# Performance work log

Hardware: AMD Instinct MI355X
Metric: run time of the kernel (lower is better)

Reference implementation:

```python
import jax, jax.numpy as jnp
import numpy as np

N_HEADS = 32
N_KV_HEADS = 8
HEAD_DIM = 128


def setup_inputs() -> dict:
    key = jax.random.key(0)
    ks = jax.random.split(key, 7)
    B, S, D = 2, 2048, 4096
    scale = 0.02
    x = jax.random.normal(ks[0], (B, S, D), dtype=jnp.float32)
    wq = jax.random.normal(ks[1], (D, D), dtype=jnp.float32) * scale
    wk = jax.random.normal(ks[2], (N_KV_HEADS * HEAD_DIM, D), dtype=jnp.float32) * scale
    wv = jax.random.normal(ks[3], (N_KV_HEADS * HEAD_DIM, D), dtype=jnp.float32) * scale
    wo = jax.random.normal(ks[4], (D, D), dtype=jnp.float32) * scale
    # RoPE frequencies: theta = 10000^{-2i/d}, angles = pos * theta
    inv_freq = 1.0 / (10000.0 ** (jnp.arange(0, HEAD_DIM, 2, dtype=jnp.float32) / HEAD_DIM))
    angles = jnp.arange(S, dtype=jnp.float32)[:, None] * inv_freq[None, :]  # (S, HEAD_DIM//2)
    freqs_cos = jnp.cos(angles)
    freqs_sin = jnp.sin(angles)
    # causal additive mask (0 on/below diagonal, -inf above)
    neg_inf = jnp.finfo(jnp.float32).min
    mask = jnp.where(jnp.triu(jnp.ones((S, S), dtype=bool), k=1), neg_inf, 0.0)[None, None]
    return {"x": x, "wq": wq, "wk": wk, "wv": wv, "wo": wo,
            "freqs_cos": freqs_cos, "freqs_sin": freqs_sin, "mask": mask,
            "start_pos": 0}


def _apply_rope(t, cos, sin):
    # t: (B, S, H, D); cos/sin: (S, D//2) -> broadcast (1, S, 1, D//2)
    b, s, h, d = t.shape
    tr = t.reshape(b, s, h, d // 2, 2)
    te, to = tr[..., 0], tr[..., 1]
    c = cos[None, :, None, :]
    si = sin[None, :, None, :]
    out = jnp.stack([te * c - to * si, te * si + to * c], axis=-1)
    return out.reshape(b, s, h, d)


def reference(x, wq, wk, wv, wo, freqs_cos, freqs_sin, mask, start_pos):
    b, s, d = x.shape
    n_rep = N_HEADS // N_KV_HEADS
    xq = (x @ wq.T).reshape(b, s, N_HEADS, HEAD_DIM)
    xk = (x @ wk.T).reshape(b, s, N_KV_HEADS, HEAD_DIM)
    xv = (x @ wv.T).reshape(b, s, N_KV_HEADS, HEAD_DIM)
    xq = _apply_rope(xq, freqs_cos, freqs_sin)
    xk = _apply_rope(xk, freqs_cos, freqs_sin)
    # repeat_kv: (B, S, Hkv, D) -> (B, S, Hkv*n_rep, D)
    keys = jnp.broadcast_to(xk[:, :, :, None, :], (b, s, N_KV_HEADS, n_rep, HEAD_DIM)).reshape(b, s, N_HEADS, HEAD_DIM)
    values = jnp.broadcast_to(xv[:, :, :, None, :], (b, s, N_KV_HEADS, n_rep, HEAD_DIM)).reshape(b, s, N_HEADS, HEAD_DIM)
    q = xq.transpose(0, 2, 1, 3)       # (B, H, S, D)
    k = keys.transpose(0, 2, 1, 3)
    v = values.transpose(0, 2, 1, 3)
    scores = jnp.einsum("bhqd,bhkd->bhqk", q, k) / np.sqrt(HEAD_DIM).astype(np.float32)
    scores = scores + mask
    probs = jax.nn.softmax(scores.astype(jnp.float32), axis=-1).astype(q.dtype)
    out = jnp.einsum("bhqk,bhkd->bhqd", probs, v)
    out = out.transpose(0, 2, 1, 3).reshape(b, s, N_HEADS * HEAD_DIM)
    return out @ wo.T
```

## Files before the change

kernel.cpp:

```cpp
#include <hip/hip_runtime.h>
#include <cstdint>
#include <cstddef>

#define B_  2
#define S_  2048
#define D_  4096
#define NH  32
#define NKV 8
#define HD  128

typedef unsigned short u16;
typedef unsigned int   u32;
typedef __attribute__((ext_vector_type(8))) short short8;
typedef __attribute__((ext_vector_type(4))) float f32x4;
typedef __attribute__((ext_vector_type(4))) u32   u32x4;

__device__ __forceinline__ u16 f2bf(float f) {
  u32 u = __float_as_uint(f);
  u32 r = (u + 0x7FFFu + ((u >> 16) & 1u)) >> 16;
  return (u16)r;
}
__device__ __forceinline__ float bf2f(u32 lo16) {
  return __uint_as_float(lo16 << 16);
}
__device__ __forceinline__ u32 cvtpk_bf16(float lo, float hi) {
  u32 r;
  asm("v_cvt_pk_bf16_f32 %0, %1, %2" : "=v"(r) : "v"(lo), "v"(hi));
  return r;
}
__device__ __forceinline__ short8 u32x4_to_short8(u32x4 v) {
  union { u32x4 a; short8 b; } u; u.a = v; return u.b;
}
__device__ __forceinline__ void load_lds16(const void* g, void* lds) {
  __builtin_amdgcn_global_load_lds(
      (const __attribute__((address_space(1))) u32*)g,
      (__attribute__((address_space(3))) u32*)lds, 16, 0, 0);
}

__global__ __launch_bounds__(256) void cvt_all(
    const float* __restrict__ x, const float* __restrict__ wq,
    const float* __restrict__ wk, const float* __restrict__ wv,
    const float* __restrict__ wo, u16* __restrict__ Xb, u16* __restrict__ Wqb,
    u16* __restrict__ Wkb, u16* __restrict__ Wvb, u16* __restrict__ Wob) {
  long i = (long)blockIdx.x * 256 + threadIdx.x;
  const float* src; u16* dst; long off;
  if (i < 2097152L)      { src = x;  dst = Xb;  off = i; }
  else if (i < 4194304L) { src = wq; dst = Wqb; off = i - 2097152L; }
  else if (i < 4718592L) { src = wk; dst = Wkb; off = i - 4194304L; }
  else if (i < 5242880L) { src = wv; dst = Wvb; off = i - 4718592L; }
  else                   { src = wo; dst = Wob; off = i - 5242880L; }
  const float4* s = (const float4*)src + off * 2;
  float4 a = s[0], b = s[1];
  uint4 o;
  o.x = (u32)f2bf(a.x) | ((u32)f2bf(a.y) << 16);
  o.y = (u32)f2bf(a.z) | ((u32)f2bf(a.w) << 16);
  o.z = (u32)f2bf(b.x) | ((u32)f2bf(b.y) << 16);
  o.w = (u32)f2bf(b.z) | ((u32)f2bf(b.w) << 16);
  *((uint4*)dst + off) = o;
}

template <int MODE, bool ROPE>
__global__ __launch_bounds__(512, 2)
void gemm256(const u16* __restrict__ A, const u16* __restrict__ Bw,
             void* __restrict__ Cout, int M, int N, int K, int Hh,
             const float* __restrict__ fc, const float* __restrict__ fs) {
  const int tid = threadIdx.x, lid = tid & 63, w = tid >> 6;
  const int lr = lid & 15, lg = lid >> 4;
  const int wm = w >> 2, wn = w & 3;

  int lin = blockIdx.y * gridDim.x + blockIdx.x;
  int bm, bn;
  if (gridDim.x == 16 && gridDim.y == 16) {
    int xcd = lin & 7, idx = lin >> 3;
    bm = ((xcd & 3) * 4 + (idx >> 3)) * 256;
    bn = ((xcd >> 2) * 8 + (idx & 7)) * 256;
  } else {
    bm = blockIdx.y * 256;
    bn = blockIdx.x * 256;
  }

  __shared__ __align__(16) u16 Al[2][2][128 * 64];
  __shared__ __align__(16) u16 Bl[2][2][128 * 64];

  f32x4 acc[8][4];
#pragma unroll
  for (int i = 0; i < 8; ++i)
#pragma unroll
    for (int j = 0; j < 4; ++j) acc[i][j] = (f32x4){0.f, 0.f, 0.f, 0.f};

#define STG_AQ(BUF, QH, KT)                                                    \
  do {                                                                         \
    _Pragma("unroll")                                                          \
    for (int j_ = 0; j_ < 2; ++j_) {                                           \
      int c_ = j_ * 512 + tid;                                                 \
      int idx_ = c_ >> 3, cb_ = c_ & 7;                                        \
      int sr_ = bm + ((idx_ & 64) << 1) + (QH) * 64 + (idx_ & 63);             \
      int sc_ = (cb_ ^ idx_) & 7;                                              \
      load_lds16(A + (size_t)sr_ * K + (KT) + sc_ * 8, &Al[BUF][QH][c_ * 8]);  \
    }                                                                          \
  } while (0)
#define STG_BN(BUF, NHh, KT)                                                   \
  do {                                                                         \
    _Pragma("unroll")                                                          \
    for (int j_ = 0; j_ < 2; ++j_) {                                           \
      int c_ = j_ * 512 + tid;                                                 \
      int idx_ = c_ >> 3, cb_ = c_ & 7;                                        \
      int sr_ = bn + ((idx_ & 96) << 1) + (NHh) * 32 + (idx_ & 31);            \
      int sc_ = (cb_ ^ idx_) & 7;                                              \
      load_lds16(Bw + (size_t)sr_ * K + (KT) + sc_ * 8, &Bl[BUF][NHh][c_ * 8]);\
    }                                                                          \
  } while (0)
#define READ_AQ(BUF, MH)                                                       \
  do {                                                                         \
    _Pragma("unroll")                                                          \
    for (int mi_ = 0; mi_ < 4; ++mi_) {                                        \
      int ix_ = wm * 64 + mi_ * 16 + lr;                                       \
      _Pragma("unroll")                                                        \
      for (int ks_ = 0; ks_ < 2; ++ks_)                                        \
        aq[mi_][ks_] = *(const short8*)&Al[BUF][MH]                            \
            [ix_ * 64 + (((ks_ * 4 + lg) ^ ix_) & 7) * 8];                     \
    }                                                                          \
  } while (0)
#define READ_BN(BUF, NHh, ARR)                                                 \
  do {                                                                         \
    _Pragma("unroll")                                                          \
    for (int ni_ = 0; ni_ < 2; ++ni_) {                                        \
      int ix_ = wn * 32 + ni_ * 16 + lr;                                       \
      _Pragma("unroll")                                                        \
      for (int ks_ = 0; ks_ < 2; ++ks_)                                        \
        ARR[ni_][ks_] = *(const short8*)&Bl[BUF][NHh]                          \
            [ix_ * 64 + (((ks_ * 4 + lg) ^ ix_) & 7) * 8];                     \
    }                                                                          \
  } while (0)
#define MFMA16(MH, NHh, ARR)                                                   \
  do {                                                                         \
    __builtin_amdgcn_s_setprio(1);                                             \
    _Pragma("unroll")                                                          \
    for (int ks_ = 0; ks_ < 2; ++ks_)                                          \
      _Pragma("unroll")                                                        \
      for (int mi_ = 0; mi_ < 4; ++mi_)                                        \
        _Pragma("unroll")                                                      \
        for (int ni_ = 0; ni_ < 2; ++ni_)                                      \
          acc[(MH) * 4 + mi_][(NHh) * 2 + ni_] =                               \
              __builtin_amdgcn_mfma_f32_16x16x32_bf16(                         \
                  aq[mi_][ks_], ARR[ni_][ks_],                                 \
                  acc[(MH) * 4 + mi_][(NHh) * 2 + ni_], 0, 0, 0);              \
    __builtin_amdgcn_s_setprio(0);                                             \
  } while (0)
#define BAR()   __builtin_amdgcn_s_barrier()
#define SCHED0() __builtin_amdgcn_sched_barrier(0)
#define LGKM0() asm volatile("s_waitcnt lgkmcnt(0)" ::: "memory")

  const int nt = K >> 6;
  const int niter = nt >> 1;

  STG_AQ(0, 0, 0); STG_BN(0, 0, 0); STG_BN(0, 1, 0); STG_AQ(0, 1, 0);
  STG_AQ(1, 0, 64); STG_BN(1, 0, 64); STG_BN(1, 1, 64);
  asm volatile("s_waitcnt vmcnt(6)" ::: "memory");
  BAR();

  short8 aq[4][2], bn0[2][2], bn1[2][2];
  for (int j = 0; j < niter; ++j) {
    const bool pf = (j + 1 < niter);
    const int k1 = (2 * j + 1) << 6, k2 = (2 * j + 2) << 6, k3 = (2 * j + 3) << 6;

    READ_AQ(0, 0); READ_BN(0, 0, bn0);
    STG_AQ(1, 1, k1);
    SCHED0(); BAR(); LGKM0(); SCHED0();
    MFMA16(0, 0, bn0); BAR();

    READ_BN(0, 1, bn1);
    if (pf) STG_AQ(0, 0, k2);
    SCHED0(); BAR(); LGKM0(); SCHED0();
    MFMA16(0, 1, bn1); BAR();

    READ_AQ(0, 1);
    if (pf) STG_BN(0, 0, k2);
    SCHED0(); BAR(); LGKM0(); SCHED0();
    MFMA16(1, 0, bn0); BAR();

    if (pf) STG_BN(0, 1, k2);
    SCHED0(); BAR(); LGKM0(); SCHED0();
    MFMA16(1, 1, bn1);
    if (pf) asm volatile("s_waitcnt vmcnt(6)" ::: "memory");
    else    asm volatile("s_waitcnt vmcnt(0)" ::: "memory");
    BAR();

    READ_AQ(1, 0); READ_BN(1, 0, bn0);
    if (pf) STG_AQ(0, 1, k2);
    SCHED0(); BAR(); LGKM0(); SCHED0();
    MFMA16(0, 0, bn0); BAR();

    READ_BN(1, 1, bn1);
    if (pf) STG_AQ(1, 0, k3);
    SCHED0(); BAR(); LGKM0(); SCHED0();
    MFMA16(0, 1, bn1); BAR();

    READ_AQ(1, 1);
    if (pf) STG_BN(1, 0, k3);
    SCHED0(); BAR(); LGKM0(); SCHED0();
    MFMA16(1, 0, bn0); BAR();

    if (pf) STG_BN(1, 1, k3);
    SCHED0(); BAR(); LGKM0(); SCHED0();
    MFMA16(1, 1, bn1);
    if (pf) {
      asm volatile("s_waitcnt vmcnt(6)" ::: "memory");
      BAR();
    }
  }
#undef STG_AQ
#undef STG_BN
#undef READ_AQ
#undef READ_BN
#undef MFMA16
#undef BAR
#undef SCHED0
#undef LGKM0

#pragma unroll
  for (int mi = 0; mi < 8; ++mi)
#pragma unroll
    for (int ni = 0; ni < 4; ++ni)
#pragma unroll
      for (int v = 0; v < 4; ++v) {
        int m = bm + wm * 128 + mi * 16 + lg * 4 + v;
        int n = bn + wn * 64 + ni * 16 + lr;
        float val = acc[mi][ni][v];
        if (ROPE) {
          int srow = m & (S_ - 1);
          int j = (n & (HD - 1)) >> 1;
          float c = fc[(size_t)srow * 64 + j];
          float s = fs[(size_t)srow * 64 + j];
          float partner = __shfl_xor(val, 1);
          val = (n & 1) ? (val * c + partner * s) : (val * c - partner * s);
          val *= (0.08838834764831845f * 1.44269504088896340f);
        }
        if (MODE == 0) {
          ((float*)Cout)[(size_t)m * N + n] = val;
        } else if (MODE == 1) {
          int b = m >> 11, s = m & (S_ - 1), hh = n >> 7, d = n & (HD - 1);
          ((u16*)Cout)[(((size_t)(b * Hh + hh)) * S_ + s) * HD + d] = f2bf(val);
        } else {
          int b = m >> 11, s = m & (S_ - 1), hh = n >> 7, d = n & (HD - 1);
          ((u16*)Cout)[(((size_t)(b * Hh + hh)) * HD + d) * S_ + s] = f2bf(val);
        }
      }
}

__global__ __launch_bounds__(256)
void gemm_kv(const u16* __restrict__ Xb, const u16* __restrict__ Wk,
             const u16* __restrict__ Wv, u16* __restrict__ Kr, u16* __restrict__ Vt,
             const float* __restrict__ fc, const float* __restrict__ fs) {
  const int tid = threadIdx.x;
  const int lid = tid & 63, w = tid >> 6;
  const int lr = lid & 15, lg = lid >> 4;
  const int wm = w >> 1, wn = w & 1;
  const int zz = blockIdx.z;
  const u16* Bw = zz ? Wv : Wk;
  const int K = D_;

  const int gx = gridDim.x;
  const int nwg = gx * gridDim.y;
  const int lin = blockIdx.y * gx + blockIdx.x;
  const int cpx = nwg >> 3;
  const int lin2 = (lin & 7) * cpx + (lin >> 3);
  const int bm = (lin2 / gx) * 128, bn = (lin2 % gx) * 128;

  __shared__ __align__(16) u16 Al[128 * 64];
  __shared__ __align__(16) u16 Bl[128 * 64];
  f32x4 acc[4][4];
#pragma unroll
  for (int i = 0; i < 4; ++i)
#pragma unroll
    for (int j = 0; j < 4; ++j) acc[i][j] = (f32x4){0.f, 0.f, 0.f, 0.f};

  for (int k0 = 0; k0 < K; k0 += 64) {
    __syncthreads();
#pragma unroll
    for (int i = 0; i < 4; ++i) {
      int c = i * 256 + tid;
      int row = c >> 3, cb = c & 7;
      int cbs = (cb ^ row) & 7;
      load_lds16(Xb + (size_t)(bm + row) * K + k0 + cbs * 8, &Al[c * 8]);
    }
#pragma unroll
    for (int i = 0; i < 4; ++i) {
      int c = i * 256 + tid;
      int row = c >> 3, cb = c & 7;
      int cbs = (cb ^ row) & 7;
      load_lds16(Bw + (size_t)(bn + row) * K + k0 + cbs * 8, &Bl[c * 8]);
    }
    __syncthreads();
#pragma unroll
    for (int ks = 0; ks < 2; ++ks) {
      short8 af[4], bf[4];
#pragma unroll
      for (int mi = 0; mi < 4; ++mi) {
        int row = wm * 64 + mi * 16 + lr;
        af[mi] = *(const short8*)&Al[row * 64 + (((ks * 4 + lg) ^ row) & 7) * 8];
      }
#pragma unroll
      for (int ni = 0; ni < 4; ++ni) {
        int row = wn * 64 + ni * 16 + lr;
        bf[ni] = *(const short8*)&Bl[row * 64 + (((ks * 4 + lg) ^ row) & 7) * 8];
      }
#pragma unroll
      for (int mi = 0; mi < 4; ++mi)
#pragma unroll
        for (int ni = 0; ni < 4; ++ni)
          acc[mi][ni] = __builtin_amdgcn_mfma_f32_16x16x32_bf16(af[mi], bf[ni], acc[mi][ni], 0, 0, 0);
    }
  }
#pragma unroll
  for (int mi = 0; mi < 4; ++mi)
#pragma unroll
    for (int ni = 0; ni < 4; ++ni)
#pragma unroll
      for (int v = 0; v < 4; ++v) {
        int m = bm + wm * 64 + mi * 16 + lg * 4 + v;
        int n = bn + wn * 64 + ni * 16 + lr;
        float val = acc[mi][ni][v];
        int b = m >> 11, s = m & (S_ - 1), hh = n >> 7, d = n & (HD - 1);
        if (zz == 0) {
          int j = d >> 1;
          float c = fc[(size_t)s * 64 + j];
          float sn = fs[(size_t)s * 64 + j];
          float partner = __shfl_xor(val, 1);
          val = (n & 1) ? (val * c + partner * sn) : (val * c - partner * sn);
          Kr[(((size_t)(b * NKV + hh)) * S_ + s) * HD + d] = f2bf(val);
        } else {
          int x = s & 31;
          int sp = (s & ~31) | (((x >> 2) & 3) * 8 + ((x >> 4) & 1) * 4 + (x & 3));
          Vt[(((size_t)(b * NKV + hh)) * HD + d) * S_ + sp] = f2bf(val);
        }
      }
}

__global__ __launch_bounds__(512, 4)
void attn_k(const u16* __restrict__ Qr, const u16* __restrict__ Kr,
            const u16* __restrict__ Vt, u16* __restrict__ Ao) {
  const int xp = blockIdx.x, h = blockIdx.y, b = blockIdx.z;
  const int kvh = h >> 2;
  const int tid = threadIdx.x, lid = tid & 63, w = tid >> 6;
  const int lr = lid & 15, lg = lid >> 4;
  __shared__ __align__(16) u16 Kl[2][64 * 128];
  __shared__ __align__(16) u16 Vl[2][128 * 64];

  const size_t qbase = ((size_t)(b * NH + h)) * S_ * HD;
  const size_t kbase = ((size_t)(b * NKV + kvh)) * S_ * HD;
  const size_t vbase = ((size_t)(b * NKV + kvh)) * HD * S_;

#define STAGE(BUF, KT)                                                              \
  do {                                                                              \
    _Pragma("unroll")                                                               \
    for (int i_ = 0; i_ < 2; ++i_) {                                                \
      int c_ = i_ * 512 + tid;                                                      \
      int row_ = c_ >> 4, cb_ = c_ & 15;                                            \
      int cbs_ = (cb_ & 8) | ((cb_ ^ row_) & 7);                                    \
      load_lds16(&Kr[kbase + (size_t)((KT) + row_) * HD + cbs_ * 8],                \
                 &Kl[BUF][(i_ * 512 + w * 64) * 8]);                                \
    }                                                                               \
    _Pragma("unroll")                                                               \
    for (int i_ = 0; i_ < 2; ++i_) {                                                \
      int c_ = i_ * 512 + tid;                                                      \
      int d_ = c_ >> 3, cb_ = c_ & 7;                                               \
      int cbs_ = (cb_ ^ d_) & 7;                                                    \
      load_lds16(&Vt[vbase + (size_t)d_ * S_ + (KT) + cbs_ * 8],                    \
                 &Vl[BUF][(i_ * 512 + w * 64) * 8]);                                \
    }                                                                               \
  } while (0)

  for (int part = 0; part < 2; ++part) {
    const int qi = part ? xp : (15 - xp);
    const int qb = qi * 128;
    const int ntiles = qi * 2 + 2;
    const int q_abs = qb + w * 16 + lr;

    short8 qf[4];
#pragma unroll
    for (int ks = 0; ks < 4; ++ks)
      qf[ks] = *(const short8*)&Qr[qbase + (size_t)q_abs * HD + ks * 32 + lg * 8];

    float m2 = -3.0e38f, osum = 0.f;
    f32x4 oacc[8];
#pragma unroll
    for (int nd = 0; nd < 8; ++nd) oacc[nd] = (f32x4){0.f, 0.f, 0.f, 0.f};

    STAGE(0, 0);
    __syncthreads();
    int cur = 0;

    for (int t = 0; t < ntiles; ++t) {
      const int kt = t * 64;
      if (t + 1 < ntiles) STAGE(cur ^ 1, kt + 64);

      f32x4 sc[4];
#pragma unroll
      for (int ni = 0; ni < 4; ++ni) sc[ni] = (f32x4){0.f, 0.f, 0.f, 0.f};
      __builtin_amdgcn_s_setprio(1);
#pragma unroll
      for (int ks = 0; ks < 4; ++ks) {
#pragma unroll
        for (int ni = 0; ni < 4; ++ni) {
          int row = ni * 16 + lr;
          int ch = ks * 4 + lg;
          int chs = (ch & 8) | ((ch ^ row) & 7);
          short8 kf = *(const short8*)&Kl[cur][row * 128 + chs * 8];
          sc[ni] = __builtin_amdgcn_mfma_f32_16x16x32_bf16(kf, qf[ks], sc[ni], 0, 0, 0);
        }
      }
      __builtin_amdgcn_s_setprio(0);

      const bool edge = (kt + 64 > qb);
      if (edge) {
#pragma unroll
        for (int ni = 0; ni < 4; ++ni)
#pragma unroll
          for (int v = 0; v < 4; ++v) {
            int kv = kt + ni * 16 + lg * 4 + v;
            if (kv > q_abs) sc[ni][v] = -3.0e38f;
          }
      }
      float mab = fmaxf(fmaxf(fmaxf(sc[0][0], sc[0][1]), fmaxf(sc[0][2], sc[0][3])),
                        fmaxf(fmaxf(sc[1][0], sc[1][1]), fmaxf(sc[1][2], sc[1][3])));
      float mcd = fmaxf(fmaxf(fmaxf(sc[2][0], sc[2][1]), fmaxf(sc[2][2], sc[2][3])),
                        fmaxf(fmaxf(sc[3][0], sc[3][1]), fmaxf(sc[3][2], sc[3][3])));
      float mx = fmaxf(mab, mcd);
      mx = fmaxf(mx, __shfl_xor(mx, 16));
      mx = fmaxf(mx, __shfl_xor(mx, 32));

      if (__any(mx > m2 + 8.0f)) {
        float mnew = fmaxf(m2, mx);
        float fr = exp2f(m2 - mnew);
        m2 = mnew;
        osum *= fr;
#pragma unroll
        for (int nd = 0; nd < 8; ++nd) oacc[nd] *= fr;
      }

      u32x4 pw0, pw1;
      float ps = 0.f;
#pragma unroll
      for (int ni = 0; ni < 4; ++ni) {
#pragma unroll
        for (int p = 0; p < 2; ++p) {
          float e0 = exp2f(sc[ni][2 * p] - m2);
          float e1 = exp2f(sc[ni][2 * p + 1] - m2);
          ps += e0 + e1;
          u32 pk = cvtpk_bf16(e0, e1);
          if (ni < 2) pw0[(ni & 1) * 2 + p] = pk;
          else        pw1[(ni & 1) * 2 + p] = pk;
        }
      }
      osum += ps;
      const short8 pf0 = u32x4_to_short8(pw0);
      const short8 pf1 = u32x4_to_short8(pw1);

      __builtin_amdgcn_s_setprio(1);
#pragma unroll
      for (int ks = 0; ks < 2; ++ks) {
        const short8 pfk = ks ? pf1 : pf0;
#pragma unroll
        for (int nd = 0; nd < 8; ++nd) {
          int rowv = nd * 16 + lr;
          int ch = ks * 4 + lg;
          short8 vf = *(const short8*)&Vl[cur][rowv * 64 + ((ch ^ rowv) & 7) * 8];
          oacc[nd] = __builtin_amdgcn_mfma_f32_16x16x32_bf16(vf, pfk, oacc[nd], 0, 0, 0);
        }
      }
      __builtin_amdgcn_s_setprio(0);
      __syncthreads();
      cur ^= 1;
    }

    float os = osum;
    os += __shfl_xor(os, 16);
    os += __shfl_xor(os, 32);
    const float inv = 1.0f / os;
    const size_t orow = ((size_t)(b * S_ + q_abs)) * D_ + h * HD;
    u32* AoW = (u32*)Ao;
#pragma unroll
    for (int nd = 0; nd < 8; ++nd) {
#pragma unroll
      for (int p = 0; p < 2; ++p) {
        u32 pk = cvtpk_bf16(oacc[nd][2 * p] * inv, oacc[nd][2 * p + 1] * inv);
        AoW[(orow + nd * 16 + lg * 4 + 2 * p) >> 1] = pk;
      }
    }
  }
#undef STAGE
}

extern "C" void kernel_launch(void* const* d_in, const int* in_sizes, int n_in,
                              void* d_out, int out_size, void* d_ws, size_t ws_size,
                              hipStream_t stream) {
  const float* x  = (const float*)d_in[0];
  const float* wq = (const float*)d_in[1];
  const float* wk = (const float*)d_in[2];
  const float* wv = (const float*)d_in[3];
  const float* wo = (const float*)d_in[4];
  const float* fc = (const float*)d_in[5];
  const float* fs = (const float*)d_in[6];

  const size_t SZ_X  = (size_t)B_ * S_ * D_ * 2;
  const size_t SZ_WQ = (size_t)D_ * D_ * 2;
  const size_t SZ_WK = (size_t)NKV * HD * D_ * 2;
  char* ws = (char*)d_ws;
  u16* Xb  = (u16*)(ws);
  u16* Wqb = (u16*)(ws + SZ_X);
  u16* Wkb = (u16*)(ws + SZ_X + SZ_WQ);
  u16* Wvb = (u16*)(ws + SZ_X + SZ_WQ + SZ_WK);
  u16* Wob = (u16*)(ws + SZ_X + SZ_WQ + 2 * SZ_WK);
  u16* Qr  = (u16*)(ws + SZ_X + 2 * SZ_WQ + 2 * SZ_WK);
  u16* Kr  = (u16*)(ws + 2 * SZ_X + 2 * SZ_WQ + 2 * SZ_WK);
  u16* Vt  = (u16*)(ws + 2 * SZ_X + 2 * SZ_WQ + 3 * SZ_WK);
  u16* Ao  = (u16*)(ws + 2 * SZ_X + 2 * SZ_WQ + 4 * SZ_WK);
  const size_t NEEDED = 3 * SZ_X + 2 * SZ_WQ + 4 * SZ_WK;
  if (ws_size < NEEDED) return;

  cvt_all<<<28672, 256, 0, stream>>>(x, wq, wk, wv, wo, Xb, Wqb, Wkb, Wvb, Wob);

  gemm256<1, true><<<dim3(16, 16), 512, 0, stream>>>(
      Xb, Wqb, Qr, B_ * S_, D_, D_, NH, fc, fs);
  gemm_kv<<<dim3(8, 32, 2), 256, 0, stream>>>(Xb, Wkb, Wvb, Kr, Vt, fc, fs);

  attn_k<<<dim3(8, NH, B_), 512, 0, stream>>>(Qr, Kr, Vt, Ao);

  gemm256<0, false><<<dim3(16, 16), 512, 0, stream>>>(
      Ao, Wob, d_out, B_ * S_, D_, D_, 0, nullptr, nullptr);
}
```

Before: 499.0 us.

## Process two 16-row query subtiles per warp in attention to reuse K/V fragments

Each warp now handles 32 query rows instead of 16, so the attention block covers 256 queries, and the grid is halved to 4 blocks per head. Every K and V fragment read from LDS feeds two MFMAs instead of one, halving LDS traffic and staging per query. In exchange each thread holds more registers (doubled accumulators and scores), occupancy drops to two blocks per CU, and with only 256 blocks the load balance across CUs gets coarser.

```diff
diff --git a/kernel.cpp b/kernel.cpp
--- a/kernel.cpp
+++ b/kernel.cpp
@@ -337,7 +337,7 @@
       }
 }
 
-__global__ __launch_bounds__(512, 4)
+__global__ __launch_bounds__(512, 2)
 void attn_k(const u16* __restrict__ Qr, const u16* __restrict__ Kr,
             const u16* __restrict__ Vt, u16* __restrict__ Ao) {
   const int xp = blockIdx.x, h = blockIdx.y, b = blockIdx.z;
@@ -372,20 +372,24 @@
   } while (0)
 
   for (int part = 0; part < 2; ++part) {
-    const int qi = part ? xp : (15 - xp);
-    const int qb = qi * 128;
-    const int ntiles = qi * 2 + 2;
-    const int q_abs = qb + w * 16 + lr;
-
-    short8 qf[4];
-#pragma unroll
-    for (int ks = 0; ks < 4; ++ks)
-      qf[ks] = *(const short8*)&Qr[qbase + (size_t)q_abs * HD + ks * 32 + lg * 8];
-
-    float m2 = -3.0e38f, osum = 0.f;
-    f32x4 oacc[8];
-#pragma unroll
-    for (int nd = 0; nd < 8; ++nd) oacc[nd] = (f32x4){0.f, 0.f, 0.f, 0.f};
+    const int pi = part ? xp : (7 - xp);
+    const int qb = pi * 256;
+    const int ntiles = pi * 4 + 4;
+    const int qa0 = qb + w * 32 + lr;
+
+    short8 qf[2][4];
+#pragma unroll
+    for (int mi = 0; mi < 2; ++mi)
+#pragma unroll
+      for (int ks = 0; ks < 4; ++ks)
+        qf[mi][ks] = *(const short8*)&Qr[qbase + (size_t)(qa0 + mi * 16) * HD + ks * 32 + lg * 8];
+
+    float m2[2] = {-3.0e38f, -3.0e38f}, osum[2] = {0.f, 0.f};
+    f32x4 oacc[2][8];
+#pragma unroll
+    for (int mi = 0; mi < 2; ++mi)
+#pragma unroll
+      for (int nd = 0; nd < 8; ++nd) oacc[mi][nd] = (f32x4){0.f, 0.f, 0.f, 0.f};
 
     STAGE(0, 0);
     __syncthreads();
@@ -395,9 +399,11 @@
       const int kt = t * 64;
       if (t + 1 < ntiles) STAGE(cur ^ 1, kt + 64);
 
-      f32x4 sc[4];
-#pragma unroll
-      for (int ni = 0; ni < 4; ++ni) sc[ni] = (f32x4){0.f, 0.f, 0.f, 0.f};
+      f32x4 sc[2][4];
+#pragma unroll
+      for (int mi = 0; mi < 2; ++mi)
+#pragma unroll
+        for (int ni = 0; ni < 4; ++ni) sc[mi][ni] = (f32x4){0.f, 0.f, 0.f, 0.f};
       __builtin_amdgcn_s_setprio(1);
 #pragma unroll
       for (int ks = 0; ks < 4; ++ks) {
@@ -407,66 +413,83 @@
           int ch = ks * 4 + lg;
           int chs = (ch & 8) | ((ch ^ row) & 7);
           short8 kf = *(const short8*)&Kl[cur][row * 128 + chs * 8];
-          sc[ni] = __builtin_amdgcn_mfma_f32_16x16x32_bf16(kf, qf[ks], sc[ni], 0, 0, 0);
+#pragma unroll
+          for (int mi = 0; mi < 2; ++mi)
+            sc[mi][ni] = __builtin_amdgcn_mfma_f32_16x16x32_bf16(kf, qf[mi][ks], sc[mi][ni], 0, 0, 0);
         }
       }
       __builtin_amdgcn_s_setprio(0);
 
       const bool edge = (kt + 64 > qb);
-      if (edge) {
-#pragma unroll
-        for (int ni = 0; ni < 4; ++ni)
-#pragma unroll
-          for (int v = 0; v < 4; ++v) {
-            int kv = kt + ni * 16 + lg * 4 + v;
-            if (kv > q_abs) sc[ni][v] = -3.0e38f;
+      float mx[2];
+#pragma unroll
+      for (int mi = 0; mi < 2; ++mi) {
+        if (edge) {
+          const int qa = qa0 + mi * 16;
+#pragma unroll
+          for (int ni = 0; ni < 4; ++ni)
+#pragma unroll
+            for (int v = 0; v < 4; ++v) {
+              int kv = kt + ni * 16 + lg * 4 + v;
+              if (kv > qa) sc[mi][ni][v] = -3.0e38f;
+            }
+        }
+        float mab = fmaxf(fmaxf(fmaxf(sc[mi][0][0], sc[mi][0][1]), fmaxf(sc[mi][0][2], sc[mi][0][3])),
+                          fmaxf(fmaxf(sc[mi][1][0], sc[mi][1][1]), fmaxf(sc[mi][1][2], sc[mi][1][3])));
+        float mcd = fmaxf(fmaxf(fmaxf(sc[mi][2][0], sc[mi][2][1]), fmaxf(sc[mi][2][2], sc[mi][2][3])),
+                          fmaxf(fmaxf(sc[mi][3][0], sc[mi][3][1]), fmaxf(sc[mi][3][2], sc[mi][3][3])));
+        float m = fmaxf(mab, mcd);
+        m = fmaxf(m, __shfl_xor(m, 16));
+        m = fmaxf(m, __shfl_xor(m, 32));
+        mx[mi] = m;
+      }
+
+      bool need = (mx[0] > m2[0] + 8.0f) || (mx[1] > m2[1] + 8.0f);
+      if (__any(need)) {
+#pragma unroll
+        for (int mi = 0; mi < 2; ++mi) {
+          float mnew = fmaxf(m2[mi], mx[mi]);
+          float fr = exp2f(m2[mi] - mnew);
+          m2[mi] = mnew;
+          osum[mi] *= fr;
+#pragma unroll
+          for (int nd = 0; nd < 8; ++nd) oacc[mi][nd] *= fr;
+        }
+      }
+
+      short8 pf[2][2];
+#pragma unroll
+      for (int mi = 0; mi < 2; ++mi) {
+        u32x4 pw0, pw1;
+        float ps = 0.f;
+#pragma unroll
+        for (int ni = 0; ni < 4; ++ni) {
+#pragma unroll
+          for (int p = 0; p < 2; ++p) {
+            float e0 = exp2f(sc[mi][ni][2 * p] - m2[mi]);
+            float e1 = exp2f(sc[mi][ni][2 * p + 1] - m2[mi]);
+            ps += e0 + e1;
+            u32 pk = cvtpk_bf16(e0, e1);
+            if (ni < 2) pw0[(ni & 1) * 2 + p] = pk;
+            else        pw1[(ni & 1) * 2 + p] = pk;
           }
-      }
-      float mab = fmaxf(fmaxf(fmaxf(sc[0][0], sc[0][1]), fmaxf(sc[0][2], sc[0][3])),
-                        fmaxf(fmaxf(sc[1][0], sc[1][1]), fmaxf(sc[1][2], sc[1][3])));
-      float mcd = fmaxf(fmaxf(fmaxf(sc[2][0], sc[2][1]), fmaxf(sc[2][2], sc[2][3])),
-                        fmaxf(fmaxf(sc[3][0], sc[3][1]), fmaxf(sc[3][2], sc[3][3])));
-      float mx = fmaxf(mab, mcd);
-      mx = fmaxf(mx, __shfl_xor(mx, 16));
-      mx = fmaxf(mx, __shfl_xor(mx, 32));
-
-      if (__any(mx > m2 + 8.0f)) {
-        float mnew = fmaxf(m2, mx);
-        float fr = exp2f(m2 - mnew);
-        m2 = mnew;
-        osum *= fr;
-#pragma unroll
-        for (int nd = 0; nd < 8; ++nd) oacc[nd] *= fr;
-      }
-
-      u32x4 pw0, pw1;
-      float ps = 0.f;
-#pragma unroll
-      for (int ni = 0; ni < 4; ++ni) {
-#pragma unroll
-        for (int p = 0; p < 2; ++p) {
-          float e0 = exp2f(sc[ni][2 * p] - m2);
-          float e1 = exp2f(sc[ni][2 * p + 1] - m2);
-          ps += e0 + e1;
-          u32 pk = cvtpk_bf16(e0, e1);
-          if (ni < 2) pw0[(ni & 1) * 2 + p] = pk;
-          else        pw1[(ni & 1) * 2 + p] = pk;
-        }
-      }
-      osum += ps;
-      const short8 pf0 = u32x4_to_short8(pw0);
-      const short8 pf1 = u32x4_to_short8(pw1);
+        }
+        osum[mi] += ps;
+        pf[mi][0] = u32x4_to_short8(pw0);
+        pf[mi][1] = u32x4_to_short8(pw1);
+      }
 
       __builtin_amdgcn_s_setprio(1);
 #pragma unroll
       for (int ks = 0; ks < 2; ++ks) {
-        const short8 pfk = ks ? pf1 : pf0;
 #pragma unroll
         for (int nd = 0; nd < 8; ++nd) {
           int rowv = nd * 16 + lr;
           int ch = ks * 4 + lg;
           short8 vf = *(const short8*)&Vl[cur][rowv * 64 + ((ch ^ rowv) & 7) * 8];
-          oacc[nd] = __builtin_amdgcn_mfma_f32_16x16x32_bf16(vf, pfk, oacc[nd], 0, 0, 0);
+#pragma unroll
+          for (int mi = 0; mi < 2; ++mi)
+            oacc[mi][nd] = __builtin_amdgcn_mfma_f32_16x16x32_bf16(vf, pf[mi][ks], oacc[mi][nd], 0, 0, 0);
         }
       }
       __builtin_amdgcn_s_setprio(0);
@@ -474,18 +497,21 @@
       cur ^= 1;
     }
 
-    float os = osum;
-    os += __shfl_xor(os, 16);
-    os += __shfl_xor(os, 32);
-    const float inv = 1.0f / os;
-    const size_t orow = ((size_t)(b * S_ + q_abs)) * D_ + h * HD;
-    u32* AoW = (u32*)Ao;
-#pragma unroll
-    for (int nd = 0; nd < 8; ++nd) {
-#pragma unroll
-      for (int p = 0; p < 2; ++p) {
-        u32 pk = cvtpk_bf16(oacc[nd][2 * p] * inv, oacc[nd][2 * p + 1] * inv);
-        AoW[(orow + nd * 16 + lg * 4 + 2 * p) >> 1] = pk;
+#pragma unroll
+    for (int mi = 0; mi < 2; ++mi) {
+      float os = osum[mi];
+      os += __shfl_xor(os, 16);
+      os += __shfl_xor(os, 32);
+      const float inv = 1.0f / os;
+      const size_t orow = ((size_t)(b * S_ + qa0 + mi * 16)) * D_ + h * HD;
+      u32* AoW = (u32*)Ao;
+#pragma unroll
+      for (int nd = 0; nd < 8; ++nd) {
+#pragma unroll
+        for (int p = 0; p < 2; ++p) {
+          u32 pk = cvtpk_bf16(oacc[mi][nd][2 * p] * inv, oacc[mi][nd][2 * p + 1] * inv);
+          AoW[(orow + nd * 16 + lg * 4 + 2 * p) >> 1] = pk;
+        }
       }
     }
   }
@@ -525,7 +551,7 @@
       Xb, Wqb, Qr, B_ * S_, D_, D_, NH, fc, fs);
   gemm_kv<<<dim3(8, 32, 2), 256, 0, stream>>>(Xb, Wkb, Wvb, Kr, Vt, fc, fs);
 
-  attn_k<<<dim3(8, NH, B_), 512, 0, stream>>>(Qr, Kr, Vt, Ao);
+  attn_k<<<dim3(4, NH, B_), 512, 0, stream>>>(Qr, Kr, Vt, Ao);
 
   gemm256<0, false><<<dim3(16, 16), 512, 0, stream>>>(
       Ao, Wob, d_out, B_ * S_, D_, D_, 0, nullptr, nullptr);
```

After: 515.2 us, median of 2. +3.2%, slower.
